# Performance work log

Hardware: AMD Instinct MI355X
Metric: run time of the kernel (lower is better)

The kernel has to match this reference:

```python
import jax, jax.numpy as jnp
import numpy as np

B, T_I, T_O, FREQ = 8192, 1440, 720, 24
TOPK = 5


def divide_no_nan(a, b):
    # a/b with NaN (0/0) and +inf (x/0) replaced by 0, matching the torch helper.
    b_safe = jnp.where(b == 0, jnp.ones_like(b), b)
    r = a / b_safe
    r = jnp.where(b == 0, jnp.zeros_like(r), r)
    return jnp.where(jnp.isnan(r) | (r == jnp.inf), jnp.zeros_like(r), r)


def setup_inputs() -> dict:
    key = jax.random.key(0)
    k1, k2, k3 = jax.random.split(key, 3)
    insample = jax.random.normal(k1, (B, T_I), dtype=jnp.float32)
    forecast = jax.random.normal(k2, (B, T_O), dtype=jnp.float32)
    target = jax.random.normal(k3, (B, T_O), dtype=jnp.float32)
    mask = jnp.ones((B, T_O), dtype=jnp.float32)
    return {"insample": insample, "freq": FREQ, "forecast": forecast,
            "target": target, "mask": mask}


def reference(insample, freq, forecast, target, mask):
    T = forecast.shape[1]
    # shape (soft-DTW-like) term: |1/T - softmax(masked error)|
    dyy = (target - forecast) * mask
    eq = jnp.abs(1.0 / T - jax.nn.softmax(dyy, axis=1))  # [B, T]
    loss_ashift = T * eq.sum(axis=1)                      # [B]

    # FFT magnitude spectra with DC bin zeroed
    forecast_f = jnp.abs(jnp.fft.rfft(forecast, axis=1)).at[:, 0].set(0.0)  # [B, F]
    target_f = jnp.abs(jnp.fft.rfft(target, axis=1)).at[:, 0].set(0.0)      # [B, F]
    Fd = target_f.shape[1]

    # Batched top-k / bottom-k gather (replaces the per-row Python loop)
    _, top_idx = jax.lax.top_k(target_f, TOPK)            # [B, 5]
    _, bot_idx = jax.lax.top_k(-target_f, Fd - TOPK)      # [B, F-5]
    tf_top = jnp.take_along_axis(target_f, top_idx, axis=1)
    ff_top = jnp.take_along_axis(forecast_f, top_idx, axis=1)
    ff_bot = jnp.take_along_axis(forecast_f, bot_idx, axis=1)
    # NOTE: computed but unused in the original forward (dead code), kept for fidelity
    loss_phase = (jnp.linalg.norm(tf_top - ff_top, axis=1)
                  + jnp.linalg.norm(ff_bot, axis=1))      # [B]

    loss_TILDEQ = 0.99 * loss_ashift

    # MASE term
    masep = jnp.mean(jnp.abs(insample[:, freq:] - insample[:, :-freq]), axis=1)  # [B]
    masked_masep_inv = divide_no_nan(mask, masep[:, None])

    # sMAPE-like term; denominator is detached (torch used .data)
    denom = jax.lax.stop_gradient(jnp.abs(forecast) + jnp.abs(target))
    smape = jnp.mean(divide_no_nan(jnp.abs(forecast - target), denom) * mask)

    return (jnp.mean(loss_TILDEQ) / 4
            + 200.0 * smape
            + jnp.mean(jnp.abs(target - forecast) * masked_masep_inv))
```

## Files before the change

### kernel.cpp

```cpp
#include <hip/hip_runtime.h>
#include <math.h>

constexpr int NB     = 8192;
constexpr int TO     = 720;
constexpr int TI     = 1440;
constexpr int FRQ    = 24;
constexpr int NV4    = TO / 4;
constexpr int NDIFF  = TI - FRQ;
constexpr int NDIFF4 = NDIFF / 4;

__device__ __forceinline__ float wredSum(float v) {
#pragma unroll
    for (int o = 32; o > 0; o >>= 1) v += __shfl_xor(v, o, 64);
    return v;
}
__device__ __forceinline__ float wredMax(float v) {
#pragma unroll
    for (int o = 32; o > 0; o >>= 1) v = fmaxf(v, __shfl_xor(v, o, 64));
    return v;
}

__device__ __forceinline__ float bredSum(float v, float* lds) {
    const int lane = threadIdx.x & 63, w = threadIdx.x >> 6;
    v = wredSum(v);
    __syncthreads();
    if (lane == 0) lds[w] = v;
    __syncthreads();
    return (lds[0] + lds[1]) + (lds[2] + lds[3]);
}
__device__ __forceinline__ float bredMax(float v, float* lds) {
    const int lane = threadIdx.x & 63, w = threadIdx.x >> 6;
    v = wredMax(v);
    __syncthreads();
    if (lane == 0) lds[w] = v;
    __syncthreads();
    return fmaxf(fmaxf(lds[0], lds[1]), fmaxf(lds[2], lds[3]));
}

__global__ __launch_bounds__(256) void tildeq_row_kernel(
    const float* __restrict__ insample,
    const float* __restrict__ forecast,
    const float* __restrict__ target,
    const float* __restrict__ mask,
    float* __restrict__ ws)
{
    __shared__ float lds[4];
    const int b = blockIdx.x;
    const int t = threadIdx.x;

    const float4* f4 = (const float4*)(forecast + (size_t)b * TO);
    const float4* g4 = (const float4*)(target   + (size_t)b * TO);
    const float4* m4 = (const float4*)(mask     + (size_t)b * TO);

    float dyy[4] = {0.f, 0.f, 0.f, 0.f};
    float smape_p = 0.f, mase_p = 0.f;
    float lmax = -INFINITY;
    const bool active = (t < NV4);

    if (active) {
        float4 fa = f4[t], ga = g4[t], ma = m4[t];
        float fv[4] = {fa.x, fa.y, fa.z, fa.w};
        float gv[4] = {ga.x, ga.y, ga.z, ga.w};
        float mv[4] = {ma.x, ma.y, ma.z, ma.w};
#pragma unroll
        for (int j = 0; j < 4; ++j) {
            float d  = gv[j] - fv[j];
            float ad = fabsf(d);
            dyy[j] = d * mv[j];
            lmax   = fmaxf(lmax, dyy[j]);
            mase_p += ad * mv[j];
            float den = fabsf(fv[j]) + fabsf(gv[j]);
            float r = (den > 0.f) ? (ad / den) : 0.f;
            if (!(r < INFINITY)) r = 0.f;
            smape_p += r * mv[j];
        }
    }

    const float4* i4 = (const float4*)(insample + (size_t)b * TI);
    float masep_p = 0.f;
    for (int idx = t; idx < NDIFF4; idx += 256) {
        float4 a = i4[idx];
        float4 c = i4[idx + FRQ / 4];
        masep_p += fabsf(c.x - a.x) + fabsf(c.y - a.y)
                 + fabsf(c.z - a.z) + fabsf(c.w - a.w);
    }

    const float rmax = bredMax(lmax, lds);
    float pexp[4];
    float sume_p = 0.f;
    if (active) {
#pragma unroll
        for (int j = 0; j < 4; ++j) { pexp[j] = __expf(dyy[j] - rmax); sume_p += pexp[j]; }
    }
    const float sume  = bredSum(sume_p,  lds);
    const float smape = bredSum(smape_p, lds);
    const float mase  = bredSum(mase_p,  lds);
    const float msum  = bredSum(masep_p, lds);

    const float inv_sume = 1.0f / sume;
    float eq_p = 0.f;
    if (active) {
#pragma unroll
        for (int j = 0; j < 4; ++j)
            eq_p += fabsf(1.0f / (float)TO - pexp[j] * inv_sume);
    }
    const float eqsum = bredSum(eq_p, lds);

    if (t == 0) {
        float masep = msum / (float)NDIFF;
        float invm  = (masep == 0.f) ? 0.f : (1.0f / masep);
        if (!(invm < INFINITY)) invm = 0.f;
        float contrib =
            (0.99f * (float)TO / (4.0f * (float)NB)) * eqsum
          + (200.0f / ((float)NB * (float)TO)) * smape
          + (1.0f  / ((float)NB * (float)TO)) * mase * invm;
        ws[b] = contrib;
    }
}

__global__ __launch_bounds__(256) void tildeq_finalize_kernel(
    const float* __restrict__ ws, float* __restrict__ out)
{
    __shared__ float lds[4];
    const float4* w4 = (const float4*)ws;
    float s = 0.f;
#pragma unroll
    for (int i = threadIdx.x; i < NB / 4; i += 256) {
        float4 v = w4[i];
        s += (v.x + v.y) + (v.z + v.w);
    }
    s = bredSum(s, lds);
    if (threadIdx.x == 0) out[0] = s;
}

extern "C" void kernel_launch(void* const* d_in, const int* in_sizes, int n_in,
                              void* d_out, int out_size, void* d_ws, size_t ws_size,
                              hipStream_t stream)
{
    const float* insample = (const float*)d_in[0];
    const float* forecast = (const float*)d_in[2];
    const float* target   = (const float*)d_in[3];
    const float* mask     = (const float*)d_in[4];
    float* ws  = (float*)d_ws;
    float* out = (float*)d_out;

    tildeq_row_kernel<<<NB, 256, 0, stream>>>(insample, forecast, target, mask, ws);
    tildeq_finalize_kernel<<<1, 256, 0, stream>>>(ws, out);
}
```

Baseline: 31.55 us.

## Map one wavefront per row and replace block reductions with shuffles

Each 256-thread block now handles four rows, one 64-lane wavefront per row. Every lane processes three float4 chunks of the row and its share of the insample range. All per-row reductions become wavefront shuffles, with the four sums fused into one shuffle loop, so the LDS traffic and six pairs of __syncthreads per row go away. The old layout left 76 of 256 threads idle on the 180-vector rows; the new one trades that for more per-lane registers and less parallelism inside each row.

Measured after the change: 27.15 us. 13.9% less time.

```diff
diff --git a/kernel.cpp b/kernel.cpp
--- a/kernel.cpp
+++ b/kernel.cpp
@@ -8,33 +8,17 @@
 constexpr int NV4    = TO / 4;
 constexpr int NDIFF  = TI - FRQ;
 constexpr int NDIFF4 = NDIFF / 4;
+constexpr int WPB    = 4;
 
-__device__ __forceinline__ float wredSum(float v) {
-#pragma unroll
-    for (int o = 32; o > 0; o >>= 1) v += __shfl_xor(v, o, 64);
-    return v;
-}
 __device__ __forceinline__ float wredMax(float v) {
 #pragma unroll
     for (int o = 32; o > 0; o >>= 1) v = fmaxf(v, __shfl_xor(v, o, 64));
     return v;
 }
-
-__device__ __forceinline__ float bredSum(float v, float* lds) {
-    const int lane = threadIdx.x & 63, w = threadIdx.x >> 6;
-    v = wredSum(v);
-    __syncthreads();
-    if (lane == 0) lds[w] = v;
-    __syncthreads();
-    return (lds[0] + lds[1]) + (lds[2] + lds[3]);
-}
-__device__ __forceinline__ float bredMax(float v, float* lds) {
-    const int lane = threadIdx.x & 63, w = threadIdx.x >> 6;
-    v = wredMax(v);
-    __syncthreads();
-    if (lane == 0) lds[w] = v;
-    __syncthreads();
-    return fmaxf(fmaxf(lds[0], lds[1]), fmaxf(lds[2], lds[3]));
+__device__ __forceinline__ float wredSum(float v) {
+#pragma unroll
+    for (int o = 32; o > 0; o >>= 1) v += __shfl_xor(v, o, 64);
+    return v;
 }
 
 __global__ __launch_bounds__(256) void tildeq_row_kernel(
@@ -44,69 +28,90 @@
     const float* __restrict__ mask,
     float* __restrict__ ws)
 {
-    __shared__ float lds[4];
-    const int b = blockIdx.x;
-    const int t = threadIdx.x;
+    const int lane = threadIdx.x & 63;
+    const int b = blockIdx.x * WPB + (threadIdx.x >> 6);
 
     const float4* f4 = (const float4*)(forecast + (size_t)b * TO);
     const float4* g4 = (const float4*)(target   + (size_t)b * TO);
     const float4* m4 = (const float4*)(mask     + (size_t)b * TO);
+    const float4* i4 = (const float4*)(insample + (size_t)b * TI);
 
-    float dyy[4] = {0.f, 0.f, 0.f, 0.f};
-    float smape_p = 0.f, mase_p = 0.f;
-    float lmax = -INFINITY;
-    const bool active = (t < NV4);
+    const bool act2 = (lane + 128) < NV4;
 
-    if (active) {
-        float4 fa = f4[t], ga = g4[t], ma = m4[t];
-        float fv[4] = {fa.x, fa.y, fa.z, fa.w};
-        float gv[4] = {ga.x, ga.y, ga.z, ga.w};
-        float mv[4] = {ma.x, ma.y, ma.z, ma.w};
+    float dyy[3][4];
+    float pexp[3][4];
+    float lmax = -INFINITY, smape_p = 0.f, mase_p = 0.f;
+
 #pragma unroll
-        for (int j = 0; j < 4; ++j) {
-            float d  = gv[j] - fv[j];
-            float ad = fabsf(d);
-            dyy[j] = d * mv[j];
-            lmax   = fmaxf(lmax, dyy[j]);
-            mase_p += ad * mv[j];
-            float den = fabsf(fv[j]) + fabsf(gv[j]);
-            float r = (den > 0.f) ? (ad / den) : 0.f;
-            if (!(r < INFINITY)) r = 0.f;
-            smape_p += r * mv[j];
+    for (int k = 0; k < 3; ++k) {
+        const int idx = lane + 64 * k;
+        const bool act = (k < 2) || act2;
+        if (act) {
+            float4 fa = f4[idx], ga = g4[idx], ma = m4[idx];
+            float fv[4] = {fa.x, fa.y, fa.z, fa.w};
+            float gv[4] = {ga.x, ga.y, ga.z, ga.w};
+            float mv[4] = {ma.x, ma.y, ma.z, ma.w};
+#pragma unroll
+            for (int j = 0; j < 4; ++j) {
+                float d  = gv[j] - fv[j];
+                float ad = fabsf(d);
+                dyy[k][j] = d * mv[j];
+                lmax = fmaxf(lmax, dyy[k][j]);
+                mase_p += ad * mv[j];
+                float den = fabsf(fv[j]) + fabsf(gv[j]);
+                float r = (den > 0.f) ? (ad / den) : 0.f;
+                if (!(r < INFINITY)) r = 0.f;
+                smape_p += r * mv[j];
+            }
+        } else {
+#pragma unroll
+            for (int j = 0; j < 4; ++j) dyy[k][j] = -INFINITY;
         }
     }
 
-    const float4* i4 = (const float4*)(insample + (size_t)b * TI);
     float masep_p = 0.f;
-    for (int idx = t; idx < NDIFF4; idx += 256) {
+    for (int idx = lane; idx < NDIFF4; idx += 64) {
         float4 a = i4[idx];
         float4 c = i4[idx + FRQ / 4];
         masep_p += fabsf(c.x - a.x) + fabsf(c.y - a.y)
                  + fabsf(c.z - a.z) + fabsf(c.w - a.w);
     }
 
-    const float rmax = bredMax(lmax, lds);
-    float pexp[4];
+    const float rmax = wredMax(lmax);
+
     float sume_p = 0.f;
-    if (active) {
 #pragma unroll
-        for (int j = 0; j < 4; ++j) { pexp[j] = __expf(dyy[j] - rmax); sume_p += pexp[j]; }
+    for (int k = 0; k < 3; ++k)
+#pragma unroll
+        for (int j = 0; j < 4; ++j) {
+            pexp[k][j] = __expf(dyy[k][j] - rmax);
+            sume_p += pexp[k][j];
+        }
+
+    float s0 = sume_p, s1 = smape_p, s2 = mase_p, s3 = masep_p;
+#pragma unroll
+    for (int o = 32; o > 0; o >>= 1) {
+        s0 += __shfl_xor(s0, o, 64);
+        s1 += __shfl_xor(s1, o, 64);
+        s2 += __shfl_xor(s2, o, 64);
+        s3 += __shfl_xor(s3, o, 64);
     }
-    const float sume  = bredSum(sume_p,  lds);
-    const float smape = bredSum(smape_p, lds);
-    const float mase  = bredSum(mase_p,  lds);
-    const float msum  = bredSum(masep_p, lds);
+    const float sume = s0, smape = s1, mase = s2, msum = s3;
 
     const float inv_sume = 1.0f / sume;
     float eq_p = 0.f;
-    if (active) {
 #pragma unroll
-        for (int j = 0; j < 4; ++j)
-            eq_p += fabsf(1.0f / (float)TO - pexp[j] * inv_sume);
+    for (int k = 0; k < 3; ++k) {
+        const bool act = (k < 2) || act2;
+        if (act) {
+#pragma unroll
+            for (int j = 0; j < 4; ++j)
+                eq_p += fabsf(1.0f / (float)TO - pexp[k][j] * inv_sume);
+        }
     }
-    const float eqsum = bredSum(eq_p, lds);
+    const float eqsum = wredSum(eq_p);
 
-    if (t == 0) {
+    if (lane == 0) {
         float masep = msum / (float)NDIFF;
         float invm  = (masep == 0.f) ? 0.f : (1.0f / masep);
         if (!(invm < INFINITY)) invm = 0.f;
@@ -122,6 +127,7 @@
     const float* __restrict__ ws, float* __restrict__ out)
 {
     __shared__ float lds[4];
+    const int lane = threadIdx.x & 63, w = threadIdx.x >> 6;
     const float4* w4 = (const float4*)ws;
     float s = 0.f;
 #pragma unroll
@@ -129,8 +135,11 @@
         float4 v = w4[i];
         s += (v.x + v.y) + (v.z + v.w);
     }
-    s = bredSum(s, lds);
-    if (threadIdx.x == 0) out[0] = s;
+    s = wredSum(s);
+    if (lane == 0) lds[w] = s;
+    __syncthreads();
+    if (threadIdx.x == 0)
+        out[0] = (lds[0] + lds[1]) + (lds[2] + lds[3]);
 }
 
 extern "C" void kernel_launch(void* const* d_in, const int* in_sizes, int n_in,
@@ -144,6 +153,6 @@
     float* ws  = (float*)d_ws;
     float* out = (float*)d_out;
 
-    tildeq_row_kernel<<<NB, 256, 0, stream>>>(insample, forecast, target, mask, ws);
+    tildeq_row_kernel<<<NB / WPB, 256, 0, stream>>>(insample, forecast, target, mask, ws);
     tildeq_finalize_kernel<<<1, 256, 0, stream>>>(ws, out);
 }
```
